# Optimization experiments

Measured on AMD Instinct MI355X. Metric: run time of the kernel, lower is better.

Reference implementation:

```python
import jax, jax.numpy as jnp
import numpy as np

BRIGHT_THRESH = 0.65
SAT_THRESH = 0.15
SMOOTH_K = 15
LAMBDA_L1 = 1.0
LAMBDA_WIN_L1 = 3.0
LAMBDA_WIN_COLOR = 1.0
WINDOW_WEIGHT = 5.0
BASE_WEIGHT = 1.0
TRANSFORM_WEIGHT = 2.0
EPS = 1e-8


def _avg_pool_same(x, k=SMOOTH_K):
    # AvgPool2d(k, stride=1, padding=k//2), count_include_pad=True (torch default)
    p = k // 2
    s = jax.lax.reduce_window(x, 0.0, jax.lax.add, (1, 1, k, k), (1, 1, 1, 1),
                              [(0, 0), (0, 0), (p, p), (p, p)])
    return s / (k * k)


def _window_detector(source):
    # Rescale from [-1,1] to [0,1] if any negative values present
    src = jnp.where(source.min() < 0, (source + 1) * 0.5, source)
    brightness = 0.299 * src[:, 0:1] + 0.587 * src[:, 1:2] + 0.114 * src[:, 2:3]
    bright_mask = jax.nn.sigmoid(20.0 * (brightness - BRIGHT_THRESH))
    saturation = src.max(axis=1, keepdims=True) - src.min(axis=1, keepdims=True)
    low_sat_mask = jax.nn.sigmoid(20.0 * (SAT_THRESH - saturation))
    return _avg_pool_same(bright_mask * low_sat_mask)


def _normalize_ch(x):
    # F.normalize over channel dim with eps clamp
    n = jnp.sqrt(jnp.sum(x * x, axis=1, keepdims=True))
    return x / jnp.maximum(n, EPS)


def setup_inputs() -> dict:
    key = jax.random.key(0)
    k1, k2, k3 = jax.random.split(key, 3)
    shape = (16, 3, 512, 512)
    return {
        "pred": jax.random.normal(k1, shape, dtype=jnp.float32),
        "target": jax.random.normal(k2, shape, dtype=jnp.float32),
        "source": jax.random.normal(k3, shape, dtype=jnp.float32),
    }


def reference(pred, target, source):
    window_mask = _window_detector(source)  # [B,1,H,W]

    # plain L1
    l1_loss = jnp.abs(pred - target).mean()

    # window-weighted L1
    weight_map = BASE_WEIGHT + (WINDOW_WEIGHT - BASE_WEIGHT) * window_mask
    win_l1_loss = (jnp.abs(pred - target) * weight_map).mean()

    # window color-transform loss
    st = target - source  # source -> target direction
    sp = pred - source    # source -> pred direction
    alignment = jnp.sum(_normalize_ch(st) * _normalize_ch(sp), axis=1, keepdims=True)
    st_mag = jnp.sqrt(jnp.sum(st * st, axis=1, keepdims=True))
    sp_mag = jnp.sqrt(jnp.sum(sp * sp, axis=1, keepdims=True))
    mag_loss = jnp.abs(sp_mag / (st_mag + EPS) - 1.0)
    color_loss = TRANSFORM_WEIGHT * (window_mask * (1.0 - alignment + 0.5 * mag_loss)).mean()

    total = LAMBDA_L1 * l1_loss + LAMBDA_WIN_L1 * win_l1_loss + LAMBDA_WIN_COLOR * color_loss
    return total
```

## Files before the change

kernel.cpp:

```cpp
#include <hip/hip_runtime.h>
#include <math.h>

#define W 512
#define H 512
#define BATCH 16
#define HW (W * H)
#define NPIX (BATCH * HW)
#define NELEM (3 * NPIX)

#define TW 64
#define TH 32
#define NBLOCKS 2048

#define MROWS 46
#define MCOLS 80
#define HCOLS 64
#define HSTRIDE 68
#define NQUAD (MROWS * 16)

__device__ __forceinline__ float fast_rcp(float x)  { return __builtin_amdgcn_rcpf(x); }
__device__ __forceinline__ float fast_sqrt(float x) { return __builtin_amdgcn_sqrtf(x); }

__device__ __forceinline__ float maskval(float r, float g, float b) {
    const float R = (r + 1.f) * 0.5f;
    const float G = (g + 1.f) * 0.5f;
    const float B = (b + 1.f) * 0.5f;
    const float bright = 0.299f * R + 0.587f * G + 0.114f * B;
    const float sat = fmaxf(R, fmaxf(G, B)) - fminf(R, fminf(G, B));
    const float bm = fast_rcp(1.f + __expf(-20.f * (bright - 0.65f)));
    const float sm = fast_rcp(1.f + __expf(-20.f * (0.15f - sat)));
    return bm * sm;
}

__global__ __launch_bounds__(256, 6) void k_fused(const float* __restrict__ pred,
                                                  const float* __restrict__ targ,
                                                  const float* __restrict__ srcp,
                                                  float* __restrict__ partials) {
    __shared__ __align__(16) float buf[MROWS * MCOLS];
    __shared__ float red[3][4];

    const int tid = threadIdx.x;
    const int bid = blockIdx.x;
    const int b  = bid >> 7;
    const int tl = bid & 127;
    const int y0 = (tl >> 3) * TH;
    const int x0 = (tl & 7) * TW;
    const size_t ibase = (size_t)b * 3 * HW;

#pragma unroll
    for (int i = 0; i < 4; ++i) {
        const int p = i * 256 + tid;
        if (p < MROWS * 20) {
            const int r = p / 20;
            const int q = p - r * 20;
            const int gy = y0 - 7 + r;
            const int gx = x0 - 8 + 4 * q;
            float4 mv = make_float4(0.f, 0.f, 0.f, 0.f);
            if ((unsigned)gy < (unsigned)H && (unsigned)gx < (unsigned)W) {
                const size_t o = ibase + (size_t)gy * W + gx;
                const float4 R4 = *(const float4*)(srcp + o);
                const float4 G4 = *(const float4*)(srcp + o + HW);
                const float4 B4 = *(const float4*)(srcp + o + 2 * HW);
                mv.x = maskval(R4.x, G4.x, B4.x);
                mv.y = maskval(R4.y, G4.y, B4.y);
                mv.z = maskval(R4.z, G4.z, B4.z);
                mv.w = maskval(R4.w, G4.w, B4.w);
            }
            *(float4*)(buf + r * MCOLS + 4 * q) = mv;
        }
    }
    __syncthreads();

    float4 hq[3];
#pragma unroll
    for (int i = 0; i < 3; ++i) {
        const int p = i * 256 + tid;
        if (p < NQUAD) {
            const int r = p >> 4;
            const int q = p & 15;
            const float* mr = buf + r * MCOLS + 4 * q;
            const float4 v0 = *(const float4*)(mr);
            const float4 v1 = *(const float4*)(mr + 4);
            const float4 v2 = *(const float4*)(mr + 8);
            const float4 v3 = *(const float4*)(mr + 12);
            const float4 v4 = *(const float4*)(mr + 16);
            const float m1 = v0.y, m2 = v0.z, m3 = v0.w;
            const float mid = v1.x + v1.y + v1.z + v1.w
                            + v2.x + v2.y + v2.z + v2.w
                            + v3.x + v3.y + v3.z + v3.w;
            const float o0 = m1 + m2 + m3 + mid;
            const float o1 = o0 - m1 + v4.x;
            const float o2 = o1 - m2 + v4.y;
            const float o3 = o2 - m3 + v4.z;
            hq[i] = make_float4(o0, o1, o2, o3);
        }
    }
    __syncthreads();
#pragma unroll
    for (int i = 0; i < 3; ++i) {
        const int p = i * 256 + tid;
        if (p < NQUAD) {
            const int r = p >> 4;
            const int q = p & 15;
            *(float4*)(buf + r * HSTRIDE + 4 * q) = hq[i];
        }
    }
    __syncthreads();

    const int cg = tid & 15;
    const int rg = tid >> 4;
    const int ro = 2 * rg;
    const size_t base0 = ibase + (size_t)(y0 + ro) * W + (x0 + 4 * cg);
    const size_t base1 = base0 + W;

    const float4 pA0 = *(const float4*)(pred + base0);
    const float4 pB0 = *(const float4*)(pred + base0 + HW);
    const float4 pC0 = *(const float4*)(pred + base0 + 2 * HW);
    const float4 tA0 = *(const float4*)(targ + base0);
    const float4 tB0 = *(const float4*)(targ + base0 + HW);
    const float4 tC0 = *(const float4*)(targ + base0 + 2 * HW);
    const float4 sA0 = *(const float4*)(srcp + base0);
    const float4 sB0 = *(const float4*)(srcp + base0 + HW);
    const float4 sC0 = *(const float4*)(srcp + base0 + 2 * HW);
    const float4 pA1 = *(const float4*)(pred + base1);
    const float4 pB1 = *(const float4*)(pred + base1 + HW);
    const float4 pC1 = *(const float4*)(pred + base1 + 2 * HW);
    const float4 tA1 = *(const float4*)(targ + base1);
    const float4 tB1 = *(const float4*)(targ + base1 + HW);
    const float4 tC1 = *(const float4*)(targ + base1 + 2 * HW);
    const float4 sA1 = *(const float4*)(srcp + base1);
    const float4 sB1 = *(const float4*)(srcp + base1 + HW);
    const float4 sC1 = *(const float4*)(srcp + base1 + 2 * HW);

    const float* hcol = buf + 4 * cg;
    float4 S0 = make_float4(0.f, 0.f, 0.f, 0.f);
#pragma unroll
    for (int k = 0; k < 15; ++k) {
        const float4 h = *(const float4*)(hcol + (ro + k) * HSTRIDE);
        S0.x += h.x; S0.y += h.y; S0.z += h.z; S0.w += h.w;
    }
    const float4 hsub = *(const float4*)(hcol + ro * HSTRIDE);
    const float4 hadd = *(const float4*)(hcol + (ro + 15) * HSTRIDE);
    const float4 S1 = make_float4(S0.x - hsub.x + hadd.x, S0.y - hsub.y + hadd.y,
                                  S0.z - hsub.z + hadd.z, S0.w - hsub.w + hadd.w);

    const float inv225 = 1.f / 225.f;
    float sA = 0.f, sAW = 0.f, sC = 0.f;

#pragma unroll
    for (int i = 0; i < 2; ++i) {
        const float4 Pv[3] = {i ? pA1 : pA0, i ? pB1 : pB0, i ? pC1 : pC0};
        const float4 Tv[3] = {i ? tA1 : tA0, i ? tB1 : tB0, i ? tC1 : tC0};
        const float4 Sv[3] = {i ? sA1 : sA0, i ? sB1 : sB0, i ? sC1 : sC0};
        const float4 Sw = i ? S1 : S0;
        const float wm[4] = {Sw.x * inv225, Sw.y * inv225, Sw.z * inv225, Sw.w * inv225};

        const float pr[4] = {Pv[0].x, Pv[0].y, Pv[0].z, Pv[0].w};
        const float pg[4] = {Pv[1].x, Pv[1].y, Pv[1].z, Pv[1].w};
        const float pb[4] = {Pv[2].x, Pv[2].y, Pv[2].z, Pv[2].w};
        const float tr[4] = {Tv[0].x, Tv[0].y, Tv[0].z, Tv[0].w};
        const float tg[4] = {Tv[1].x, Tv[1].y, Tv[1].z, Tv[1].w};
        const float tb[4] = {Tv[2].x, Tv[2].y, Tv[2].z, Tv[2].w};
        const float sr[4] = {Sv[0].x, Sv[0].y, Sv[0].z, Sv[0].w};
        const float sg[4] = {Sv[1].x, Sv[1].y, Sv[1].z, Sv[1].w};
        const float sb[4] = {Sv[2].x, Sv[2].y, Sv[2].z, Sv[2].w};

#pragma unroll
        for (int j = 0; j < 4; ++j) {
            const float a = fabsf(pr[j] - tr[j]) + fabsf(pg[j] - tg[j]) + fabsf(pb[j] - tb[j]);
            const float stx = tr[j] - sr[j], sty = tg[j] - sg[j], stz = tb[j] - sb[j];
            const float spx = pr[j] - sr[j], spy = pg[j] - sg[j], spz = pb[j] - sb[j];
            const float dot = stx * spx + sty * spy + stz * spz;
            const float stm = fast_sqrt(stx * stx + sty * sty + stz * stz);
            const float spm = fast_sqrt(spx * spx + spy * spy + spz * spz);
            const float align = dot * fast_rcp(fmaxf(stm, 1e-8f) * fmaxf(spm, 1e-8f));
            const float mag = fabsf(spm * fast_rcp(stm + 1e-8f) - 1.f);
            const float c = 1.f - align + 0.5f * mag;
            sA  += a;
            sAW += a * wm[j];
            sC  += c * wm[j];
        }
    }

#pragma unroll
    for (int off = 32; off > 0; off >>= 1) {
        sA  += __shfl_down(sA, off);
        sAW += __shfl_down(sAW, off);
        sC  += __shfl_down(sC, off);
    }
    const int lane = tid & 63;
    const int wave = tid >> 6;
    if (lane == 0) { red[0][wave] = sA; red[1][wave] = sAW; red[2][wave] = sC; }
    __syncthreads();
    if (tid == 0) {
        partials[(size_t)bid * 3 + 0] = red[0][0] + red[0][1] + red[0][2] + red[0][3];
        partials[(size_t)bid * 3 + 1] = red[1][0] + red[1][1] + red[1][2] + red[1][3];
        partials[(size_t)bid * 3 + 2] = red[2][0] + red[2][1] + red[2][2] + red[2][3];
    }
}

__global__ __launch_bounds__(256) void k_final(const float* __restrict__ partials,
                                               float* __restrict__ out) {
    double a = 0.0, aw = 0.0, c = 0.0;
    for (int i = threadIdx.x; i < NBLOCKS; i += 256) {
        a  += (double)partials[(size_t)i * 3 + 0];
        aw += (double)partials[(size_t)i * 3 + 1];
        c  += (double)partials[(size_t)i * 3 + 2];
    }
#pragma unroll
    for (int off = 32; off > 0; off >>= 1) {
        a  += __shfl_down(a, off);
        aw += __shfl_down(aw, off);
        c  += __shfl_down(c, off);
    }
    __shared__ double rd[3][4];
    const int lane = threadIdx.x & 63;
    const int wave = threadIdx.x >> 6;
    if (lane == 0) { rd[0][wave] = a; rd[1][wave] = aw; rd[2][wave] = c; }
    __syncthreads();
    if (threadIdx.x == 0) {
        const double A  = rd[0][0] + rd[0][1] + rd[0][2] + rd[0][3];
        const double AW = rd[1][0] + rd[1][1] + rd[1][2] + rd[1][3];
        const double C  = rd[2][0] + rd[2][1] + rd[2][2] + rd[2][3];
        const double N = (double)NELEM;
        const double M = (double)NPIX;
        out[0] = (float)((4.0 * A + 12.0 * AW) / N + 2.0 * C / M);
    }
}

extern "C" void kernel_launch(void* const* d_in, const int* in_sizes, int n_in,
                              void* d_out, int out_size, void* d_ws, size_t ws_size,
                              hipStream_t stream) {
    const float* pred = (const float*)d_in[0];
    const float* targ = (const float*)d_in[1];
    const float* src  = (const float*)d_in[2];

    float* partials = (float*)d_ws;

    k_fused<<<NBLOCKS, 256, 0, stream>>>(pred, targ, src, partials);
    k_final<<<1, 256, 0, stream>>>(partials, (float*)d_out);
}
```

Before: 166.9 us.

## Reuse interior source loads for mask and load halo separately, prefetch pred/target early

The interior source pixels each thread needs for the loss are now loaded once and also used to compute the window mask for the shared-memory tile. Only the halo region (408 quads) is loaded separately for the mask, so source is no longer read twice for interior pixels. Half of the pred/target loads are issued before the pooling phase to overlap latency, and the occupancy hint drops from 6 to 4 blocks per SM. The higher register pressure from holding loads across barriers may reduce occupancy.

```diff
diff --git a/kernel.cpp b/kernel.cpp
--- a/kernel.cpp
+++ b/kernel.cpp
@@ -14,9 +14,9 @@
 
 #define MROWS 46
 #define MCOLS 80
-#define HCOLS 64
 #define HSTRIDE 68
 #define NQUAD (MROWS * 16)
+#define NHALO 408
 
 __device__ __forceinline__ float fast_rcp(float x)  { return __builtin_amdgcn_rcpf(x); }
 __device__ __forceinline__ float fast_sqrt(float x) { return __builtin_amdgcn_sqrtf(x); }
@@ -32,7 +32,45 @@
     return bm * sm;
 }
 
-__global__ __launch_bounds__(256, 6) void k_fused(const float* __restrict__ pred,
+__device__ __forceinline__ float4 maskval4(float4 R4, float4 G4, float4 B4) {
+    float4 m;
+    m.x = maskval(R4.x, G4.x, B4.x);
+    m.y = maskval(R4.y, G4.y, B4.y);
+    m.z = maskval(R4.z, G4.z, B4.z);
+    m.w = maskval(R4.w, G4.w, B4.w);
+    return m;
+}
+
+__device__ __forceinline__ void loss4(const float4& pR, const float4& pG, const float4& pB,
+                                      const float4& tR, const float4& tG, const float4& tB,
+                                      const float4& sR, const float4& sG, const float4& sB,
+                                      const float4& Sw, float& sA, float& sAW, float& sC) {
+    const float inv225 = 1.f / 225.f;
+    const float wm[4] = {Sw.x * inv225, Sw.y * inv225, Sw.z * inv225, Sw.w * inv225};
+    const float pr[4] = {pR.x, pR.y, pR.z, pR.w}, pg[4] = {pG.x, pG.y, pG.z, pG.w},
+                pb[4] = {pB.x, pB.y, pB.z, pB.w};
+    const float tr[4] = {tR.x, tR.y, tR.z, tR.w}, tg[4] = {tG.x, tG.y, tG.z, tG.w},
+                tb[4] = {tB.x, tB.y, tB.z, tB.w};
+    const float sr[4] = {sR.x, sR.y, sR.z, sR.w}, sg[4] = {sG.x, sG.y, sG.z, sG.w},
+                sb[4] = {sB.x, sB.y, sB.z, sB.w};
+#pragma unroll
+    for (int j = 0; j < 4; ++j) {
+        const float a = fabsf(pr[j] - tr[j]) + fabsf(pg[j] - tg[j]) + fabsf(pb[j] - tb[j]);
+        const float stx = tr[j] - sr[j], sty = tg[j] - sg[j], stz = tb[j] - sb[j];
+        const float spx = pr[j] - sr[j], spy = pg[j] - sg[j], spz = pb[j] - sb[j];
+        const float dot = stx * spx + sty * spy + stz * spz;
+        const float stm = fast_sqrt(stx * stx + sty * sty + stz * stz);
+        const float spm = fast_sqrt(spx * spx + spy * spy + spz * spz);
+        const float align = dot * fast_rcp(fmaxf(stm, 1e-8f) * fmaxf(spm, 1e-8f));
+        const float mag = fabsf(spm * fast_rcp(stm + 1e-8f) - 1.f);
+        const float c = 1.f - align + 0.5f * mag;
+        sA  += a;
+        sAW += a * wm[j];
+        sC  += c * wm[j];
+    }
+}
+
+__global__ __launch_bounds__(256, 4) void k_fused(const float* __restrict__ pred,
                                                   const float* __restrict__ targ,
                                                   const float* __restrict__ srcp,
                                                   float* __restrict__ partials) {
@@ -47,52 +85,80 @@
     const int x0 = (tl & 7) * TW;
     const size_t ibase = (size_t)b * 3 * HW;
 
-#pragma unroll
-    for (int i = 0; i < 4; ++i) {
-        const int p = i * 256 + tid;
-        if (p < MROWS * 20) {
-            const int r = p / 20;
-            const int q = p - r * 20;
-            const int gy = y0 - 7 + r;
-            const int gx = x0 - 8 + 4 * q;
+    const int R = tid >> 4;
+    const int q = tid & 15;
+    const int yA = y0 + 2 * R;
+    const int xq = x0 + 4 * q;
+    const size_t base0 = ibase + (size_t)yA * W + xq;
+    const size_t base1 = base0 + W;
+
+    const float4 sR0 = *(const float4*)(srcp + base0);
+    const float4 sG0 = *(const float4*)(srcp + base0 + HW);
+    const float4 sB0 = *(const float4*)(srcp + base0 + 2 * HW);
+    const float4 sR1 = *(const float4*)(srcp + base1);
+    const float4 sG1 = *(const float4*)(srcp + base1 + HW);
+    const float4 sB1 = *(const float4*)(srcp + base1 + 2 * HW);
+    const float4 pR0 = *(const float4*)(pred + base0);
+    const float4 pG0 = *(const float4*)(pred + base0 + HW);
+    const float4 pB0 = *(const float4*)(pred + base0 + 2 * HW);
+    const float4 tR0 = *(const float4*)(targ + base0);
+    const float4 tG0 = *(const float4*)(targ + base0 + HW);
+    const float4 tB0 = *(const float4*)(targ + base0 + 2 * HW);
+
+#pragma unroll
+    for (int it = 0; it < 2; ++it) {
+        const int hi = it * 256 + tid;
+        if (hi < NHALO) {
+            int smr, hq;
+            if (hi < 280) {
+                const int hr = hi / 20;
+                smr = (hr < 7) ? hr : hr + 32;
+                hq  = hi - hr * 20;
+            } else {
+                const int j = hi - 280;
+                smr = (j >> 2) + 7;
+                const int k = j & 3;
+                hq  = (k < 2) ? k : k + 16;
+            }
+            const int gy = y0 - 7 + smr;
+            const int gx = x0 - 8 + 4 * hq;
             float4 mv = make_float4(0.f, 0.f, 0.f, 0.f);
             if ((unsigned)gy < (unsigned)H && (unsigned)gx < (unsigned)W) {
                 const size_t o = ibase + (size_t)gy * W + gx;
                 const float4 R4 = *(const float4*)(srcp + o);
                 const float4 G4 = *(const float4*)(srcp + o + HW);
                 const float4 B4 = *(const float4*)(srcp + o + 2 * HW);
-                mv.x = maskval(R4.x, G4.x, B4.x);
-                mv.y = maskval(R4.y, G4.y, B4.y);
-                mv.z = maskval(R4.z, G4.z, B4.z);
-                mv.w = maskval(R4.w, G4.w, B4.w);
+                mv = maskval4(R4, G4, B4);
             }
-            *(float4*)(buf + r * MCOLS + 4 * q) = mv;
+            *(float4*)(buf + smr * MCOLS + 4 * hq) = mv;
         }
     }
-    __syncthreads();
-
-    float4 hq[3];
+    *(float4*)(buf + (2 * R + 7) * MCOLS + 8 + 4 * q) = maskval4(sR0, sG0, sB0);
+    *(float4*)(buf + (2 * R + 8) * MCOLS + 8 + 4 * q) = maskval4(sR1, sG1, sB1);
+    __syncthreads();
+
+    float4 hq3[3];
 #pragma unroll
     for (int i = 0; i < 3; ++i) {
         const int p = i * 256 + tid;
         if (p < NQUAD) {
-            const int r = p >> 4;
-            const int q = p & 15;
-            const float* mr = buf + r * MCOLS + 4 * q;
+            const int r  = p >> 4;
+            const int qq = p & 15;
+            const float* mr = buf + r * MCOLS + 4 * qq;
             const float4 v0 = *(const float4*)(mr);
             const float4 v1 = *(const float4*)(mr + 4);
             const float4 v2 = *(const float4*)(mr + 8);
             const float4 v3 = *(const float4*)(mr + 12);
             const float4 v4 = *(const float4*)(mr + 16);
-            const float m1 = v0.y, m2 = v0.z, m3 = v0.w;
             const float mid = v1.x + v1.y + v1.z + v1.w
                             + v2.x + v2.y + v2.z + v2.w
                             + v3.x + v3.y + v3.z + v3.w;
-            const float o0 = m1 + m2 + m3 + mid;
-            const float o1 = o0 - m1 + v4.x;
-            const float o2 = o1 - m2 + v4.y;
-            const float o3 = o2 - m3 + v4.z;
-            hq[i] = make_float4(o0, o1, o2, o3);
+            float4 h;
+            h.x = v0.y + v0.z + v0.w + mid;
+            h.y = h.x - v0.y + v4.x;
+            h.z = h.y - v0.z + v4.y;
+            h.w = h.z - v0.w + v4.z;
+            hq3[i] = h;
         }
     }
     __syncthreads();
@@ -100,87 +166,35 @@
     for (int i = 0; i < 3; ++i) {
         const int p = i * 256 + tid;
         if (p < NQUAD) {
-            const int r = p >> 4;
-            const int q = p & 15;
-            *(float4*)(buf + r * HSTRIDE + 4 * q) = hq[i];
+            const int r  = p >> 4;
+            const int qq = p & 15;
+            *(float4*)(buf + r * HSTRIDE + 4 * qq) = hq3[i];
         }
     }
     __syncthreads();
 
-    const int cg = tid & 15;
-    const int rg = tid >> 4;
-    const int ro = 2 * rg;
-    const size_t base0 = ibase + (size_t)(y0 + ro) * W + (x0 + 4 * cg);
-    const size_t base1 = base0 + W;
-
-    const float4 pA0 = *(const float4*)(pred + base0);
-    const float4 pB0 = *(const float4*)(pred + base0 + HW);
-    const float4 pC0 = *(const float4*)(pred + base0 + 2 * HW);
-    const float4 tA0 = *(const float4*)(targ + base0);
-    const float4 tB0 = *(const float4*)(targ + base0 + HW);
-    const float4 tC0 = *(const float4*)(targ + base0 + 2 * HW);
-    const float4 sA0 = *(const float4*)(srcp + base0);
-    const float4 sB0 = *(const float4*)(srcp + base0 + HW);
-    const float4 sC0 = *(const float4*)(srcp + base0 + 2 * HW);
-    const float4 pA1 = *(const float4*)(pred + base1);
-    const float4 pB1 = *(const float4*)(pred + base1 + HW);
-    const float4 pC1 = *(const float4*)(pred + base1 + 2 * HW);
-    const float4 tA1 = *(const float4*)(targ + base1);
-    const float4 tB1 = *(const float4*)(targ + base1 + HW);
-    const float4 tC1 = *(const float4*)(targ + base1 + 2 * HW);
-    const float4 sA1 = *(const float4*)(srcp + base1);
-    const float4 sB1 = *(const float4*)(srcp + base1 + HW);
-    const float4 sC1 = *(const float4*)(srcp + base1 + 2 * HW);
-
-    const float* hcol = buf + 4 * cg;
+    const float4 pR1 = *(const float4*)(pred + base1);
+    const float4 pG1 = *(const float4*)(pred + base1 + HW);
+    const float4 pB1 = *(const float4*)(pred + base1 + 2 * HW);
+    const float4 tR1 = *(const float4*)(targ + base1);
+    const float4 tG1 = *(const float4*)(targ + base1 + HW);
+    const float4 tB1 = *(const float4*)(targ + base1 + 2 * HW);
+
+    const float* hcol = buf + 4 * q;
     float4 S0 = make_float4(0.f, 0.f, 0.f, 0.f);
 #pragma unroll
     for (int k = 0; k < 15; ++k) {
-        const float4 h = *(const float4*)(hcol + (ro + k) * HSTRIDE);
+        const float4 h = *(const float4*)(hcol + (2 * R + k) * HSTRIDE);
         S0.x += h.x; S0.y += h.y; S0.z += h.z; S0.w += h.w;
     }
-    const float4 hsub = *(const float4*)(hcol + ro * HSTRIDE);
-    const float4 hadd = *(const float4*)(hcol + (ro + 15) * HSTRIDE);
+    const float4 hsub = *(const float4*)(hcol + (2 * R) * HSTRIDE);
+    const float4 hadd = *(const float4*)(hcol + (2 * R + 15) * HSTRIDE);
     const float4 S1 = make_float4(S0.x - hsub.x + hadd.x, S0.y - hsub.y + hadd.y,
                                   S0.z - hsub.z + hadd.z, S0.w - hsub.w + hadd.w);
 
-    const float inv225 = 1.f / 225.f;
     float sA = 0.f, sAW = 0.f, sC = 0.f;
-
-#pragma unroll
-    for (int i = 0; i < 2; ++i) {
-        const float4 Pv[3] = {i ? pA1 : pA0, i ? pB1 : pB0, i ? pC1 : pC0};
-        const float4 Tv[3] = {i ? tA1 : tA0, i ? tB1 : tB0, i ? tC1 : tC0};
-        const float4 Sv[3] = {i ? sA1 : sA0, i ? sB1 : sB0, i ? sC1 : sC0};
-        const float4 Sw = i ? S1 : S0;
-        const float wm[4] = {Sw.x * inv225, Sw.y * inv225, Sw.z * inv225, Sw.w * inv225};
-
-        const float pr[4] = {Pv[0].x, Pv[0].y, Pv[0].z, Pv[0].w};
-        const float pg[4] = {Pv[1].x, Pv[1].y, Pv[1].z, Pv[1].w};
-        const float pb[4] = {Pv[2].x, Pv[2].y, Pv[2].z, Pv[2].w};
-        const float tr[4] = {Tv[0].x, Tv[0].y, Tv[0].z, Tv[0].w};
-        const float tg[4] = {Tv[1].x, Tv[1].y, Tv[1].z, Tv[1].w};
-        const float tb[4] = {Tv[2].x, Tv[2].y, Tv[2].z, Tv[2].w};
-        const float sr[4] = {Sv[0].x, Sv[0].y, Sv[0].z, Sv[0].w};
-        const float sg[4] = {Sv[1].x, Sv[1].y, Sv[1].z, Sv[1].w};
-        const float sb[4] = {Sv[2].x, Sv[2].y, Sv[2].z, Sv[2].w};
-
-#pragma unroll
-        for (int j = 0; j < 4; ++j) {
-            const float a = fabsf(pr[j] - tr[j]) + fabsf(pg[j] - tg[j]) + fabsf(pb[j] - tb[j]);
-            const float stx = tr[j] - sr[j], sty = tg[j] - sg[j], stz = tb[j] - sb[j];
-            const float spx = pr[j] - sr[j], spy = pg[j] - sg[j], spz = pb[j] - sb[j];
-            const float dot = stx * spx + sty * spy + stz * spz;
-            const float stm = fast_sqrt(stx * stx + sty * sty + stz * stz);
-            const float spm = fast_sqrt(spx * spx + spy * spy + spz * spz);
-            const float align = dot * fast_rcp(fmaxf(stm, 1e-8f) * fmaxf(spm, 1e-8f));
-            const float mag = fabsf(spm * fast_rcp(stm + 1e-8f) - 1.f);
-            const float c = 1.f - align + 0.5f * mag;
-            sA  += a;
-            sAW += a * wm[j];
-            sC  += c * wm[j];
-        }
-    }
+    loss4(pR0, pG0, pB0, tR0, tG0, tB0, sR0, sG0, sB0, S0, sA, sAW, sC);
+    loss4(pR1, pG1, pB1, tR1, tG1, tB1, sR1, sG1, sB1, S1, sA, sAW, sC);
 
 #pragma unroll
     for (int off = 32; off > 0; off >>= 1) {
```

Measured after the change: 161.5 us. 1.03x faster.
